# Performance work log

Hardware: AMD Instinct MI355X
Metric: run time of the kernel (lower is better)

Reference implementation:

```python
import jax, jax.numpy as jnp
import numpy as np

E, K, D_IN, D_H, D_OUT, B = 16, 2, 256, 512, 256, 32768


def setup_inputs() -> dict:
    key = jax.random.key(0)
    ks = jax.random.split(key, 7)
    s_in = 1.0 / np.sqrt(D_IN)
    s_h = 1.0 / np.sqrt(D_H)
    return {
        "x": jax.random.normal(ks[0], (B, D_IN), jnp.float32),
        "Wg": jax.random.normal(ks[1], (D_IN, E), jnp.float32) * s_in,
        "bg": jnp.zeros((E,), jnp.float32),
        "W1": jax.random.normal(ks[2], (E, D_IN, D_H), jnp.float32) * s_in,
        "b1": jnp.zeros((E, D_H), jnp.float32),
        "W2": jax.random.normal(ks[3], (E, D_H, D_OUT), jnp.float32) * s_h,
        "b2": jnp.zeros((E, D_OUT), jnp.float32),
    }


def reference(x, Wg, bg, W1, b1, W2, b2):
    # Gating: softmax over experts, top-k, renormalize routing weights.
    probs = jax.nn.softmax(x @ Wg + bg, axis=-1)            # [B, E]
    top_vals, top_idx = jax.lax.top_k(probs, K)              # [B, K]
    w = top_vals / jnp.sum(top_vals, axis=-1, keepdims=True)  # [B, K]

    # Dense per-expert MLP over all tokens (vectorized dispatch equivalent).
    h = jax.nn.relu(jnp.einsum("bi,eih->ebh", x, W1) + b1[:, None, :])  # [E, B, Dh]
    out_e = jnp.einsum("ebh,eho->ebo", h, W2) + b2[:, None, :]          # [E, B, Do]

    # Gather each token's k assigned expert outputs and combine weighted.
    out_be = jnp.transpose(out_e, (1, 0, 2))                  # [B, E, Do]
    sel = jnp.take_along_axis(out_be, top_idx[:, :, None], axis=1)  # [B, K, Do]
    return jnp.sum(w[:, :, None] * sel, axis=1)               # [B, Do]
```

## Files before the change

### kernel.cpp

```cpp
#include <hip/hip_runtime.h>

#define E_ 16
#define DIN 256
#define DH 512
#define DOUT 256
#define BTOK 32768

typedef _Float16 half8 __attribute__((ext_vector_type(8)));
typedef _Float16 half4v __attribute__((ext_vector_type(4)));
typedef float float4v __attribute__((ext_vector_type(4)));

#define OFF_P1      0u
#define OFF_P2      4194304u
#define OFF_XH      8388608u
#define OFF_SCR     25165824u
#define OFF_TIDX    58720256u
#define OFF_TW      58982400u
#define OFF_STOK    59244544u
#define OFF_SW      59506688u
#define OFF_APOS    59768832u
#define OFF_CNT     60030976u
#define OFF_OFFS    60031104u
#define OFF_CUR     60031232u

__global__ __launch_bounds__(64) void pack_kernel(const float* __restrict__ W1,
                                                  const float* __restrict__ W2,
                                                  _Float16* __restrict__ p1,
                                                  _Float16* __restrict__ p2) {
    int bid = blockIdx.x;
    int l = threadIdx.x;
    int quad = l >> 4, l15 = l & 15;
    if (bid < 4096) {
        int nt = bid & 31, kt = (bid >> 5) & 7, e = bid >> 8;
        half8 v;
#pragma unroll
        for (int j = 0; j < 8; ++j)
            v[j] = (_Float16)W1[(e * DIN + kt * 32 + quad * 8 + j) * DH + nt * 16 + l15];
        ((half8*)p1)[bid * 64 + l] = v;
    } else {
        int b2i = bid - 4096;
        int nt = b2i & 15, kt = (b2i >> 4) & 15, e = b2i >> 8;
        half8 v;
#pragma unroll
        for (int j = 0; j < 8; ++j)
            v[j] = (_Float16)W2[(e * DH + kt * 32 + quad * 8 + j) * DOUT + nt * 16 + l15];
        ((half8*)p2)[b2i * 64 + l] = v;
    }
}

__global__ __launch_bounds__(256) void xbf_kernel(const float* __restrict__ x,
                                                  _Float16* __restrict__ xh,
                                                  int* __restrict__ counts) {
    int g = blockIdx.x * 256 + threadIdx.x;
    float4v a = ((const float4v*)x)[2 * g];
    float4v b = ((const float4v*)x)[2 * g + 1];
    half8 v;
#pragma unroll
    for (int j = 0; j < 4; ++j) { v[j] = (_Float16)a[j]; v[4 + j] = (_Float16)b[j]; }
    ((half8*)xh)[g] = v;
    if (blockIdx.x == 0 && threadIdx.x < 16) counts[threadIdx.x] = 0;
}

__global__ __launch_bounds__(256) void gate_kernel(const float* __restrict__ x,
                                                   const float* __restrict__ Wg,
                                                   const float* __restrict__ bg,
                                                   int* __restrict__ tidx,
                                                   float* __restrict__ tw,
                                                   int* __restrict__ counts) {
    __shared__ float WgS[DIN * E_];
    __shared__ int hcnt[16];
    int tid = threadIdx.x;
    if (tid < 16) hcnt[tid] = 0;
#pragma unroll
    for (int i = 0; i < 4; ++i)
        ((float4v*)WgS)[tid + i * 256] = ((const float4v*)Wg)[tid + i * 256];
    __syncthreads();

    int tl = tid >> 2, q = tid & 3;
    int b = blockIdx.x * 64 + tl;
    const float* xr = x + b * DIN + q * 64;

    float acc[16];
#pragma unroll
    for (int e = 0; e < 16; ++e) acc[e] = 0.f;

    for (int ii = 0; ii < 16; ++ii) {
        float4v xv = ((const float4v*)xr)[ii];
#pragma unroll
        for (int j = 0; j < 4; ++j) {
            const float4v* wrow = (const float4v*)&WgS[(q * 64 + ii * 4 + j) * 16];
            float xs = xv[j];
#pragma unroll
            for (int e4 = 0; e4 < 4; ++e4) {
                float4v w4 = wrow[e4];
                acc[e4 * 4 + 0] += xs * w4[0];
                acc[e4 * 4 + 1] += xs * w4[1];
                acc[e4 * 4 + 2] += xs * w4[2];
                acc[e4 * 4 + 3] += xs * w4[3];
            }
        }
    }
#pragma unroll
    for (int e = 0; e < 16; ++e) {
        acc[e] += __shfl_xor(acc[e], 1);
        acc[e] += __shfl_xor(acc[e], 2);
    }
    if (q == 0) {
        float m1 = -3.4e38f, m2 = -3.4e38f;
        int i1 = 0, i2 = 0;
#pragma unroll
        for (int e = 0; e < 16; ++e) {
            float v = acc[e] + bg[e];
            if (v > m1) { m2 = m1; i2 = i1; m1 = v; i1 = e; }
            else if (v > m2) { m2 = v; i2 = e; }
        }
        float e2 = __expf(m2 - m1);
        float w1 = 1.f / (1.f + e2);
        tidx[b * 2] = i1; tidx[b * 2 + 1] = i2;
        tw[b * 2] = w1;  tw[b * 2 + 1] = e2 * w1;
        atomicAdd(&hcnt[i1], 1);
        atomicAdd(&hcnt[i2], 1);
    }
    __syncthreads();
    if (tid < 16) atomicAdd(&counts[tid], hcnt[tid]);
}

__global__ void scan_kernel(const int* __restrict__ counts, int* __restrict__ offsets,
                            int* __restrict__ cursor) {
    if (threadIdx.x == 0) {
        int run = 0;
        for (int e = 0; e < 16; ++e) { offsets[e] = run; cursor[e] = run; run += counts[e]; }
        offsets[16] = run;
    }
}

__global__ __launch_bounds__(256) void scatter_kernel(const int* __restrict__ tidx,
                                                      const float* __restrict__ tw,
                                                      int* __restrict__ cursor,
                                                      int* __restrict__ stok,
                                                      float* __restrict__ sw,
                                                      int* __restrict__ apos) {
    __shared__ int lc[16];
    __shared__ int lbase[16];
    int tid = threadIdx.x;
    if (tid < 16) lc[tid] = 0;
    __syncthreads();
    int g = blockIdx.x * 256 + tid;
    int e = tidx[g];
    int rank = atomicAdd(&lc[e], 1);
    __syncthreads();
    if (tid < 16) lbase[tid] = atomicAdd(&cursor[tid], lc[tid]);
    __syncthreads();
    int pos = lbase[e] + rank;
    stok[pos] = g >> 1;
    sw[pos] = tw[g];
    apos[g] = pos;
}

__device__ __forceinline__ int hsw(int row, int col) {
    return row * 512 + ((((col >> 3) ^ (row & 7)) << 3) | (col & 7));
}

__global__ __launch_bounds__(256, 2) void mlp_kernel(const _Float16* __restrict__ xh,
                                                     const _Float16* __restrict__ p1,
                                                     const _Float16* __restrict__ p2,
                                                     const float* __restrict__ b1,
                                                     const float* __restrict__ b2,
                                                     const int* __restrict__ offsets,
                                                     const int* __restrict__ stok,
                                                     const float* __restrict__ sw,
                                                     _Float16* __restrict__ scr) {
    __shared__ _Float16 Hs[64 * 512];
    const int e = blockIdx.y;
    const int off = offsets[e];
    const int ne = offsets[e + 1] - off;
    const int ts = blockIdx.x * 64;
    if (ts >= ne) return;
    const int rows = min(64, ne - ts);
    const int tid = threadIdx.x;
    const int wv = tid >> 6;
    const int l = tid & 63;
    const int l15 = l & 15;
    const int quad = l >> 4;

    const _Float16* xp[4];
#pragma unroll
    for (int mt = 0; mt < 4; ++mt) {
        int r = mt * 16 + l15; if (r >= rows) r = rows - 1;
        xp[mt] = xh + stok[off + ts + r] * DIN + quad * 8;
    }

    const half8* p1b = (const half8*)p1;
    const half8* p2b = (const half8*)p2;

    float4v acc1[4][8];
#pragma unroll
    for (int mt = 0; mt < 4; ++mt)
#pragma unroll
        for (int nt = 0; nt < 8; ++nt) acc1[mt][nt] = (float4v){0.f, 0.f, 0.f, 0.f};

#pragma unroll
    for (int kt = 0; kt < 8; ++kt) {
        half8 af[4];
#pragma unroll
        for (int mt = 0; mt < 4; ++mt) af[mt] = *(const half8*)(xp[mt] + kt * 32);
#pragma unroll
        for (int nt = 0; nt < 8; ++nt) {
            half8 bf = p1b[((e * 8 + kt) * 32 + wv * 8 + nt) * 64 + l];
#pragma unroll
            for (int mt = 0; mt < 4; ++mt)
                acc1[mt][nt] = __builtin_amdgcn_mfma_f32_16x16x32_f16(af[mt], bf, acc1[mt][nt], 0, 0, 0);
        }
    }
#pragma unroll
    for (int nt = 0; nt < 8; ++nt) {
        float b1v = b1[e * DH + (wv * 8 + nt) * 16 + l15];
        int col = (wv * 8 + nt) * 16 + l15;
#pragma unroll
        for (int mt = 0; mt < 4; ++mt)
#pragma unroll
            for (int r = 0; r < 4; ++r) {
                float v = acc1[mt][nt][r] + b1v;
                Hs[hsw(mt * 16 + quad * 4 + r, col)] = (_Float16)(v > 0.f ? v : 0.f);
            }
    }
    __syncthreads();

    float4v acc2[4][4];
#pragma unroll
    for (int mt = 0; mt < 4; ++mt)
#pragma unroll
        for (int nt = 0; nt < 4; ++nt) acc2[mt][nt] = (float4v){0.f, 0.f, 0.f, 0.f};

#pragma unroll
    for (int kt2 = 0; kt2 < 16; ++kt2) {
        half8 af2[4];
#pragma unroll
        for (int mt = 0; mt < 4; ++mt) {
            int row = mt * 16 + l15;
            int chunk = (kt2 * 4 + quad) ^ (row & 7);
            af2[mt] = *(const half8*)&Hs[row * 512 + chunk * 8];
        }
#pragma unroll
        for (int nt = 0; nt < 4; ++nt) {
            half8 bf2 = p2b[((e * 16 + kt2) * 16 + wv * 4 + nt) * 64 + l];
#pragma unroll
            for (int mt = 0; mt < 4; ++mt)
                acc2[mt][nt] = __builtin_amdgcn_mfma_f32_16x16x32_f16(af2[mt], bf2, acc2[mt][nt], 0, 0, 0);
        }
    }

#pragma unroll
    for (int mt = 0; mt < 4; ++mt)
#pragma unroll
        for (int r = 0; r < 4; ++r) {
            int rg = mt * 16 + quad * 4 + r;
            if (rg < rows) {
                int pos = off + ts + rg;
                float wt = sw[pos];
#pragma unroll
                for (int nt = 0; nt < 4; ++nt) {
                    int col = (wv * 4 + nt) * 16 + l15;
                    scr[pos * DOUT + col] = (_Float16)(wt * (acc2[mt][nt][r] + b2[e * DOUT + col]));
                }
            }
        }
}

__global__ __launch_bounds__(256) void combine_kernel(const _Float16* __restrict__ scr,
                                                      const int* __restrict__ apos,
                                                      float* __restrict__ out) {
    int wv = threadIdx.x >> 6;
    int l = threadIdx.x & 63;
    int t = blockIdx.x * 4 + wv;
    int p0 = apos[2 * t], p1 = apos[2 * t + 1];
    half4v a = *(const half4v*)(scr + p0 * DOUT + l * 4);
    half4v b = *(const half4v*)(scr + p1 * DOUT + l * 4);
    float4v o;
#pragma unroll
    for (int j = 0; j < 4; ++j) o[j] = (float)a[j] + (float)b[j];
    ((float4v*)(out + t * DOUT))[l] = o;
}

extern "C" void kernel_launch(void* const* d_in, const int* in_sizes, int n_in,
                              void* d_out, int out_size, void* d_ws, size_t ws_size,
                              hipStream_t stream) {
    const float* x  = (const float*)d_in[0];
    const float* Wg = (const float*)d_in[1];
    const float* bg = (const float*)d_in[2];
    const float* W1 = (const float*)d_in[3];
    const float* b1 = (const float*)d_in[4];
    const float* W2 = (const float*)d_in[5];
    const float* b2 = (const float*)d_in[6];
    float* out = (float*)d_out;

    char* ws = (char*)d_ws;
    _Float16* p1  = (_Float16*)(ws + OFF_P1);
    _Float16* p2  = (_Float16*)(ws + OFF_P2);
    _Float16* xh  = (_Float16*)(ws + OFF_XH);
    _Float16* scr = (_Float16*)(ws + OFF_SCR);
    int* tidx     = (int*)(ws + OFF_TIDX);
    float* tw     = (float*)(ws + OFF_TW);
    int* stok     = (int*)(ws + OFF_STOK);
    float* swp    = (float*)(ws + OFF_SW);
    int* apos     = (int*)(ws + OFF_APOS);
    int* counts   = (int*)(ws + OFF_CNT);
    int* offsets  = (int*)(ws + OFF_OFFS);
    int* cursor   = (int*)(ws + OFF_CUR);

    pack_kernel<<<dim3(8192), dim3(64), 0, stream>>>(W1, W2, p1, p2);
    xbf_kernel<<<dim3(4096), dim3(256), 0, stream>>>(x, xh, counts);
    gate_kernel<<<dim3(512), dim3(256), 0, stream>>>(x, Wg, bg, tidx, tw, counts);
    scan_kernel<<<dim3(1), dim3(64), 0, stream>>>(counts, offsets, cursor);
    scatter_kernel<<<dim3(256), dim3(256), 0, stream>>>(tidx, tw, cursor, stok, swp, apos);
    mlp_kernel<<<dim3(512, 16), dim3(256), 0, stream>>>(xh, p1, p2, b1, b2, offsets,
                                                        stok, swp, scr);
    combine_kernel<<<dim3(8192), dim3(256), 0, stream>>>(scr, apos, out);
}
```

Baseline: 230.9 us.

## Fuse x conversion into gating, compact MoE tile grid, restructure MLP waves

```diff
diff --git a/kernel.cpp b/kernel.cpp
--- a/kernel.cpp
+++ b/kernel.cpp
@@ -5,6 +5,7 @@
 #define DH 512
 #define DOUT 256
 #define BTOK 32768
+#define HPAD 520
 
 typedef _Float16 half8 __attribute__((ext_vector_type(8)));
 typedef _Float16 half4v __attribute__((ext_vector_type(4)));
@@ -18,52 +19,44 @@
 #define OFF_TW      58982400u
 #define OFF_STOK    59244544u
 #define OFF_SW      59506688u
-#define OFF_APOS    59768832u
-#define OFF_CNT     60030976u
-#define OFF_OFFS    60031104u
-#define OFF_CUR     60031232u
-
-__global__ __launch_bounds__(64) void pack_kernel(const float* __restrict__ W1,
-                                                  const float* __restrict__ W2,
-                                                  _Float16* __restrict__ p1,
-                                                  _Float16* __restrict__ p2) {
-    int bid = blockIdx.x;
-    int l = threadIdx.x;
+#define OFF_CNT     59768832u
+#define OFF_OFFS    59768960u
+#define OFF_CUR     59769088u
+#define OFF_TMAP    59769216u
+#define OFF_TMC     59773504u
+
+__global__ __launch_bounds__(256) void pack_kernel(const float* __restrict__ W1,
+                                                   const float* __restrict__ W2,
+                                                   _Float16* __restrict__ p1,
+                                                   _Float16* __restrict__ p2,
+                                                   int* __restrict__ counts) {
+    int tid = threadIdx.x;
+    int bid = blockIdx.x * 4 + (tid >> 6);
+    int l = tid & 63;
     int quad = l >> 4, l15 = l & 15;
+    if (blockIdx.x == 0 && tid < 16) counts[tid] = 0;
     if (bid < 4096) {
-        int nt = bid & 31, kt = (bid >> 5) & 7, e = bid >> 8;
+        int ht = bid & 31, kt = (bid >> 5) & 7, e = bid >> 8;
         half8 v;
 #pragma unroll
         for (int j = 0; j < 8; ++j)
-            v[j] = (_Float16)W1[(e * DIN + kt * 32 + quad * 8 + j) * DH + nt * 16 + l15];
+            v[j] = (_Float16)W1[(e * DIN + kt * 32 + quad * 8 + j) * DH + ht * 16 + l15];
         ((half8*)p1)[bid * 64 + l] = v;
     } else {
         int b2i = bid - 4096;
-        int nt = b2i & 15, kt = (b2i >> 4) & 15, e = b2i >> 8;
+        int ot = b2i & 15, kt = (b2i >> 4) & 15, e = b2i >> 8;
         half8 v;
 #pragma unroll
         for (int j = 0; j < 8; ++j)
-            v[j] = (_Float16)W2[(e * DH + kt * 32 + quad * 8 + j) * DOUT + nt * 16 + l15];
+            v[j] = (_Float16)W2[(e * DH + kt * 32 + quad * 8 + j) * DOUT + ot * 16 + l15];
         ((half8*)p2)[b2i * 64 + l] = v;
     }
-}
-
-__global__ __launch_bounds__(256) void xbf_kernel(const float* __restrict__ x,
-                                                  _Float16* __restrict__ xh,
-                                                  int* __restrict__ counts) {
-    int g = blockIdx.x * 256 + threadIdx.x;
-    float4v a = ((const float4v*)x)[2 * g];
-    float4v b = ((const float4v*)x)[2 * g + 1];
-    half8 v;
-#pragma unroll
-    for (int j = 0; j < 4; ++j) { v[j] = (_Float16)a[j]; v[4 + j] = (_Float16)b[j]; }
-    ((half8*)xh)[g] = v;
-    if (blockIdx.x == 0 && threadIdx.x < 16) counts[threadIdx.x] = 0;
 }
 
 __global__ __launch_bounds__(256) void gate_kernel(const float* __restrict__ x,
                                                    const float* __restrict__ Wg,
                                                    const float* __restrict__ bg,
+                                                   _Float16* __restrict__ xh,
                                                    int* __restrict__ tidx,
                                                    float* __restrict__ tw,
                                                    int* __restrict__ counts) {
@@ -76,61 +69,99 @@
         ((float4v*)WgS)[tid + i * 256] = ((const float4v*)Wg)[tid + i * 256];
     __syncthreads();
 
-    int tl = tid >> 2, q = tid & 3;
-    int b = blockIdx.x * 64 + tl;
-    const float* xr = x + b * DIN + q * 64;
-
-    float acc[16];
-#pragma unroll
-    for (int e = 0; e < 16; ++e) acc[e] = 0.f;
-
-    for (int ii = 0; ii < 16; ++ii) {
-        float4v xv = ((const float4v*)xr)[ii];
+    int q = tid & 7, tg = tid >> 3;
+    int t0 = blockIdx.x * 64 + tg * 2;
+
+    float acc[2][16];
+#pragma unroll
+    for (int tt = 0; tt < 2; ++tt)
+#pragma unroll
+        for (int e = 0; e < 16; ++e) acc[tt][e] = 0.f;
+
+#pragma unroll
+    for (int ii = 0; ii < 8; ++ii) {
+        int kb = q * 32 + ii * 4;
+        float4v xv[2];
+#pragma unroll
+        for (int tt = 0; tt < 2; ++tt) {
+            xv[tt] = *(const float4v*)&x[(t0 + tt) * DIN + kb];
+            half4v hv;
+#pragma unroll
+            for (int j = 0; j < 4; ++j) hv[j] = (_Float16)xv[tt][j];
+            *(half4v*)&xh[(t0 + tt) * DIN + kb] = hv;
+        }
 #pragma unroll
         for (int j = 0; j < 4; ++j) {
-            const float4v* wrow = (const float4v*)&WgS[(q * 64 + ii * 4 + j) * 16];
-            float xs = xv[j];
-#pragma unroll
-            for (int e4 = 0; e4 < 4; ++e4) {
-                float4v w4 = wrow[e4];
-                acc[e4 * 4 + 0] += xs * w4[0];
-                acc[e4 * 4 + 1] += xs * w4[1];
-                acc[e4 * 4 + 2] += xs * w4[2];
-                acc[e4 * 4 + 3] += xs * w4[3];
+            const float4v* wrow = (const float4v*)&WgS[(kb + j) * 16];
+            float4v w0 = wrow[0], w1 = wrow[1], w2 = wrow[2], w3 = wrow[3];
+#pragma unroll
+            for (int tt = 0; tt < 2; ++tt) {
+                float xs = xv[tt][j];
+#pragma unroll
+                for (int c = 0; c < 4; ++c) {
+                    acc[tt][0 + c]  += xs * w0[c];
+                    acc[tt][4 + c]  += xs * w1[c];
+                    acc[tt][8 + c]  += xs * w2[c];
+                    acc[tt][12 + c] += xs * w3[c];
+                }
             }
         }
     }
 #pragma unroll
-    for (int e = 0; e < 16; ++e) {
-        acc[e] += __shfl_xor(acc[e], 1);
-        acc[e] += __shfl_xor(acc[e], 2);
-    }
+    for (int tt = 0; tt < 2; ++tt)
+#pragma unroll
+        for (int e = 0; e < 16; ++e) {
+            acc[tt][e] += __shfl_xor(acc[tt][e], 1);
+            acc[tt][e] += __shfl_xor(acc[tt][e], 2);
+            acc[tt][e] += __shfl_xor(acc[tt][e], 4);
+        }
     if (q == 0) {
-        float m1 = -3.4e38f, m2 = -3.4e38f;
-        int i1 = 0, i2 = 0;
-#pragma unroll
+#pragma unroll
+        for (int tt = 0; tt < 2; ++tt) {
+            int b = t0 + tt;
+            float m1 = -3.4e38f, m2 = -3.4e38f;
+            int i1 = 0, i2 = 0;
+#pragma unroll
+            for (int e = 0; e < 16; ++e) {
+                float v = acc[tt][e] + bg[e];
+                if (v > m1) { m2 = m1; i2 = i1; m1 = v; i1 = e; }
+                else if (v > m2) { m2 = v; i2 = e; }
+            }
+            float e2 = __expf(m2 - m1);
+            float w1 = 1.f / (1.f + e2);
+            tidx[b * 2] = i1; tidx[b * 2 + 1] = i2;
+            tw[b * 2] = w1;  tw[b * 2 + 1] = e2 * w1;
+            atomicAdd(&hcnt[i1], 1);
+            atomicAdd(&hcnt[i2], 1);
+        }
+    }
+    __syncthreads();
+    if (tid < 16) atomicAdd(&counts[tid], hcnt[tid]);
+}
+
+__global__ void scan_kernel(const int* __restrict__ counts, int* __restrict__ offsets,
+                            int* __restrict__ cursor, int* __restrict__ tmap,
+                            int* __restrict__ tmc) {
+    __shared__ int s_cnt[16];
+    __shared__ int s_tstart[17];
+    int tid = threadIdx.x;
+    if (tid == 0) {
+        int run = 0, trun = 0;
         for (int e = 0; e < 16; ++e) {
-            float v = acc[e] + bg[e];
-            if (v > m1) { m2 = m1; i2 = i1; m1 = v; i1 = e; }
-            else if (v > m2) { m2 = v; i2 = e; }
-        }
-        float e2 = __expf(m2 - m1);
-        float w1 = 1.f / (1.f + e2);
-        tidx[b * 2] = i1; tidx[b * 2 + 1] = i2;
-        tw[b * 2] = w1;  tw[b * 2 + 1] = e2 * w1;
-        atomicAdd(&hcnt[i1], 1);
-        atomicAdd(&hcnt[i2], 1);
-    }
-    __syncthreads();
-    if (tid < 16) atomicAdd(&counts[tid], hcnt[tid]);
-}
-
-__global__ void scan_kernel(const int* __restrict__ counts, int* __restrict__ offsets,
-                            int* __restrict__ cursor) {
-    if (threadIdx.x == 0) {
-        int run = 0;
-        for (int e = 0; e < 16; ++e) { offsets[e] = run; cursor[e] = run; run += counts[e]; }
+            int c = counts[e];
+            s_cnt[e] = c;
+            offsets[e] = run; cursor[e] = run; run += c;
+            s_tstart[e] = trun; trun += (c + 63) >> 6;
+        }
         offsets[16] = run;
+        s_tstart[16] = trun;
+        tmc[0] = trun;
+    }
+    __syncthreads();
+    if (tid < 16) {
+        int nt = (s_cnt[tid] + 63) >> 6;
+        int base = s_tstart[tid];
+        for (int t = 0; t < nt; ++t) tmap[base + t] = (tid << 16) | t;
     }
 }
 
@@ -138,8 +169,7 @@
                                                       const float* __restrict__ tw,
                                                       int* __restrict__ cursor,
                                                       int* __restrict__ stok,
-                                                      float* __restrict__ sw,
-                                                      int* __restrict__ apos) {
+                                                      float* __restrict__ sw) {
     __shared__ int lc[16];
     __shared__ int lbase[16];
     int tid = threadIdx.x;
@@ -152,16 +182,11 @@
     if (tid < 16) lbase[tid] = atomicAdd(&cursor[tid], lc[tid]);
     __syncthreads();
     int pos = lbase[e] + rank;
-    stok[pos] = g >> 1;
+    stok[pos] = g;
     sw[pos] = tw[g];
-    apos[g] = pos;
-}
-
-__device__ __forceinline__ int hsw(int row, int col) {
-    return row * 512 + ((((col >> 3) ^ (row & 7)) << 3) | (col & 7));
-}
-
-__global__ __launch_bounds__(256, 2) void mlp_kernel(const _Float16* __restrict__ xh,
+}
+
+__global__ __launch_bounds__(512, 4) void mlp_kernel(const _Float16* __restrict__ xh,
                                                      const _Float16* __restrict__ p1,
                                                      const _Float16* __restrict__ p2,
                                                      const float* __restrict__ b1,
@@ -169,113 +194,118 @@
                                                      const int* __restrict__ offsets,
                                                      const int* __restrict__ stok,
                                                      const float* __restrict__ sw,
+                                                     const int* __restrict__ tmap,
+                                                     const int* __restrict__ tmc,
                                                      _Float16* __restrict__ scr) {
-    __shared__ _Float16 Hs[64 * 512];
-    const int e = blockIdx.y;
+    __shared__ _Float16 Hs[64 * HPAD];
+    if ((int)blockIdx.x >= tmc[0]) return;
+    const int tile = tmap[blockIdx.x];
+    const int e = tile >> 16;
+    const int ts = (tile & 0xffff) * 64;
     const int off = offsets[e];
     const int ne = offsets[e + 1] - off;
-    const int ts = blockIdx.x * 64;
-    if (ts >= ne) return;
     const int rows = min(64, ne - ts);
+
     const int tid = threadIdx.x;
-    const int wv = tid >> 6;
+    const int w = tid >> 6;
     const int l = tid & 63;
     const int l15 = l & 15;
     const int quad = l >> 4;
 
-    const _Float16* xp[4];
-#pragma unroll
-    for (int mt = 0; mt < 4; ++mt) {
-        int r = mt * 16 + l15; if (r >= rows) r = rows - 1;
-        xp[mt] = xh + stok[off + ts + r] * DIN + quad * 8;
+    const _Float16* tb[4];
+#pragma unroll
+    for (int nt = 0; nt < 4; ++nt) {
+        int r = nt * 16 + l15; if (r >= rows) r = rows - 1;
+        tb[nt] = xh + (stok[off + ts + r] >> 1) * DIN + quad * 8;
     }
 
     const half8* p1b = (const half8*)p1;
     const half8* p2b = (const half8*)p2;
 
-    float4v acc1[4][8];
+    float4v acc1[4][4];
+#pragma unroll
+    for (int mh = 0; mh < 4; ++mh)
+#pragma unroll
+        for (int nt = 0; nt < 4; ++nt) acc1[mh][nt] = (float4v){0.f, 0.f, 0.f, 0.f};
+
+#pragma unroll
+    for (int kt = 0; kt < 8; ++kt) {
+        half8 bq[4];
+#pragma unroll
+        for (int nt = 0; nt < 4; ++nt) bq[nt] = *(const half8*)(tb[nt] + kt * 32);
+#pragma unroll
+        for (int mh = 0; mh < 4; ++mh) {
+            half8 aw = p1b[((e * 8 + kt) * 32 + w * 4 + mh) * 64 + l];
+#pragma unroll
+            for (int nt = 0; nt < 4; ++nt)
+                acc1[mh][nt] = __builtin_amdgcn_mfma_f32_16x16x32_f16(aw, bq[nt], acc1[mh][nt], 0, 0, 0);
+        }
+    }
+#pragma unroll
+    for (int mh = 0; mh < 4; ++mh) {
+        int hb = (w * 4 + mh) * 16 + quad * 4;
+        float4v b1q = *(const float4v*)&b1[e * DH + hb];
+#pragma unroll
+        for (int nt = 0; nt < 4; ++nt) {
+            half4v hv;
+#pragma unroll
+            for (int r = 0; r < 4; ++r) {
+                float v = acc1[mh][nt][r] + b1q[r];
+                hv[r] = (_Float16)(v > 0.f ? v : 0.f);
+            }
+            *(half4v*)&Hs[(nt * 16 + l15) * HPAD + hb] = hv;
+        }
+    }
+    __syncthreads();
+
+    float4v acc2[4][2];
 #pragma unroll
     for (int mt = 0; mt < 4; ++mt)
 #pragma unroll
-        for (int nt = 0; nt < 8; ++nt) acc1[mt][nt] = (float4v){0.f, 0.f, 0.f, 0.f};
-
-#pragma unroll
-    for (int kt = 0; kt < 8; ++kt) {
-        half8 af[4];
-#pragma unroll
-        for (int mt = 0; mt < 4; ++mt) af[mt] = *(const half8*)(xp[mt] + kt * 32);
-#pragma unroll
-        for (int nt = 0; nt < 8; ++nt) {
-            half8 bf = p1b[((e * 8 + kt) * 32 + wv * 8 + nt) * 64 + l];
+        for (int n = 0; n < 2; ++n) acc2[mt][n] = (float4v){0.f, 0.f, 0.f, 0.f};
+
+#pragma unroll
+    for (int kt2 = 0; kt2 < 16; ++kt2) {
+        half8 ha[4];
+#pragma unroll
+        for (int mt = 0; mt < 4; ++mt)
+            ha[mt] = *(const half8*)&Hs[(mt * 16 + l15) * HPAD + kt2 * 32 + quad * 8];
+#pragma unroll
+        for (int n = 0; n < 2; ++n) {
+            half8 bw = p2b[((e * 16 + kt2) * 16 + w * 2 + n) * 64 + l];
 #pragma unroll
             for (int mt = 0; mt < 4; ++mt)
-                acc1[mt][nt] = __builtin_amdgcn_mfma_f32_16x16x32_f16(af[mt], bf, acc1[mt][nt], 0, 0, 0);
-        }
-    }
-#pragma unroll
-    for (int nt = 0; nt < 8; ++nt) {
-        float b1v = b1[e * DH + (wv * 8 + nt) * 16 + l15];
-        int col = (wv * 8 + nt) * 16 + l15;
-#pragma unroll
-        for (int mt = 0; mt < 4; ++mt)
-#pragma unroll
-            for (int r = 0; r < 4; ++r) {
-                float v = acc1[mt][nt][r] + b1v;
-                Hs[hsw(mt * 16 + quad * 4 + r, col)] = (_Float16)(v > 0.f ? v : 0.f);
-            }
-    }
-    __syncthreads();
-
-    float4v acc2[4][4];
+                acc2[mt][n] = __builtin_amdgcn_mfma_f32_16x16x32_f16(ha[mt], bw, acc2[mt][n], 0, 0, 0);
+        }
+    }
+
+    float b2v[2];
+#pragma unroll
+    for (int n = 0; n < 2; ++n) b2v[n] = b2[e * DOUT + (w * 2 + n) * 16 + l15];
 #pragma unroll
     for (int mt = 0; mt < 4; ++mt)
 #pragma unroll
-        for (int nt = 0; nt < 4; ++nt) acc2[mt][nt] = (float4v){0.f, 0.f, 0.f, 0.f};
-
-#pragma unroll
-    for (int kt2 = 0; kt2 < 16; ++kt2) {
-        half8 af2[4];
-#pragma unroll
-        for (int mt = 0; mt < 4; ++mt) {
-            int row = mt * 16 + l15;
-            int chunk = (kt2 * 4 + quad) ^ (row & 7);
-            af2[mt] = *(const half8*)&Hs[row * 512 + chunk * 8];
-        }
-#pragma unroll
-        for (int nt = 0; nt < 4; ++nt) {
-            half8 bf2 = p2b[((e * 16 + kt2) * 16 + wv * 4 + nt) * 64 + l];
-#pragma unroll
-            for (int mt = 0; mt < 4; ++mt)
-                acc2[mt][nt] = __builtin_amdgcn_mfma_f32_16x16x32_f16(af2[mt], bf2, acc2[mt][nt], 0, 0, 0);
-        }
-    }
-
-#pragma unroll
-    for (int mt = 0; mt < 4; ++mt)
-#pragma unroll
         for (int r = 0; r < 4; ++r) {
-            int rg = mt * 16 + quad * 4 + r;
-            if (rg < rows) {
-                int pos = off + ts + rg;
-                float wt = sw[pos];
-#pragma unroll
-                for (int nt = 0; nt < 4; ++nt) {
-                    int col = (wv * 4 + nt) * 16 + l15;
-                    scr[pos * DOUT + col] = (_Float16)(wt * (acc2[mt][nt][r] + b2[e * DOUT + col]));
+            int row = mt * 16 + quad * 4 + r;
+            if (row < rows) {
+                int g = stok[off + ts + row];
+                float wt = sw[off + ts + row];
+#pragma unroll
+                for (int n = 0; n < 2; ++n) {
+                    int col = (w * 2 + n) * 16 + l15;
+                    scr[g * DOUT + col] = (_Float16)(wt * (acc2[mt][n][r] + b2v[n]));
                 }
             }
         }
 }
 
 __global__ __launch_bounds__(256) void combine_kernel(const _Float16* __restrict__ scr,
-                                                      const int* __restrict__ apos,
                                                       float* __restrict__ out) {
     int wv = threadIdx.x >> 6;
     int l = threadIdx.x & 63;
     int t = blockIdx.x * 4 + wv;
-    int p0 = apos[2 * t], p1 = apos[2 * t + 1];
-    half4v a = *(const half4v*)(scr + p0 * DOUT + l * 4);
-    half4v b = *(const half4v*)(scr + p1 * DOUT + l * 4);
+    half4v a = ((const half4v*)(scr + t * 2 * DOUT))[l];
+    half4v b = ((const half4v*)(scr + t * 2 * DOUT + DOUT))[l];
     float4v o;
 #pragma unroll
     for (int j = 0; j < 4; ++j) o[j] = (float)a[j] + (float)b[j];
@@ -303,17 +333,17 @@
     float* tw     = (float*)(ws + OFF_TW);
     int* stok     = (int*)(ws + OFF_STOK);
     float* swp    = (float*)(ws + OFF_SW);
-    int* apos     = (int*)(ws + OFF_APOS);
     int* counts   = (int*)(ws + OFF_CNT);
     int* offsets  = (int*)(ws + OFF_OFFS);
     int* cursor   = (int*)(ws + OFF_CUR);
-
-    pack_kernel<<<dim3(8192), dim3(64), 0, stream>>>(W1, W2, p1, p2);
-    xbf_kernel<<<dim3(4096), dim3(256), 0, stream>>>(x, xh, counts);
-    gate_kernel<<<dim3(512), dim3(256), 0, stream>>>(x, Wg, bg, tidx, tw, counts);
-    scan_kernel<<<dim3(1), dim3(64), 0, stream>>>(counts, offsets, cursor);
-    scatter_kernel<<<dim3(256), dim3(256), 0, stream>>>(tidx, tw, cursor, stok, swp, apos);
-    mlp_kernel<<<dim3(512, 16), dim3(256), 0, stream>>>(xh, p1, p2, b1, b2, offsets,
-                                                        stok, swp, scr);
-    combine_kernel<<<dim3(8192), dim3(256), 0, stream>>>(scr, apos, out);
-}
+    int* tmap     = (int*)(ws + OFF_TMAP);
+    int* tmc      = (int*)(ws + OFF_TMC);
+
+    pack_kernel<<<dim3(2048), dim3(256), 0, stream>>>(W1, W2, p1, p2, counts);
+    gate_kernel<<<dim3(512), dim3(256), 0, stream>>>(x, Wg, bg, xh, tidx, tw, counts);
+    scan_kernel<<<dim3(1), dim3(64), 0, stream>>>(counts, offsets, cursor, tmap, tmc);
+    scatter_kernel<<<dim3(256), dim3(256), 0, stream>>>(tidx, tw, cursor, stok, swp);
+    mlp_kernel<<<dim3(1040), dim3(512), 0, stream>>>(xh, p1, p2, b1, b2, offsets,
+                                                     stok, swp, tmap, tmc, scr);
+    combine_kernel<<<dim3(8192), dim3(256), 0, stream>>>(scr, out);
+}
```

New measurement: 228.0 us. No clear change (-1.3%).
